# Optimization experiments

Hardware: AMD Instinct MI355X
Metric: run time of the kernel (lower is better)

The kernel has to match this reference:

```python
import jax, jax.numpy as jnp
import numpy as np

OUT_FEATURES = 4096
IN_FEATURES = 4096
R = 16
DIST = 4
N_FREQ = 10000
SCALING = 150.0


def setup_inputs() -> dict:
    key = jax.random.key(0)
    k_x, k_w, k_b, k_s, k_a, k_i = jax.random.split(key, 6)
    x = jax.random.normal(k_x, (4, 2048, IN_FEATURES), dtype=jnp.float32)
    base_w = jax.random.normal(k_w, (OUT_FEATURES, IN_FEATURES), dtype=jnp.float32) * 0.02
    base_b = jax.random.normal(k_b, (OUT_FEATURES,), dtype=jnp.float32) * 0.02
    spectrum = jax.random.normal(k_s, (N_FREQ,), dtype=jnp.float32)
    hora_A = jax.random.normal(k_a, (R, IN_FEATURES), dtype=jnp.float32)
    # torch uses randperm(r*out_features)[:n_frequency] -> unique flat indices
    idx = jax.random.permutation(k_i, R * OUT_FEATURES)[:N_FREQ].astype(jnp.int32)
    return {"x": x, "base_w": base_w, "base_b": base_b,
            "spectrum": spectrum, "hora_A": hora_A, "idx": idx}


def reference(x, base_w, base_b, spectrum, hora_A, idx):
    # --- get_delta_weight ---
    rows = idx // R            # index into out_features
    cols = idx % R             # index into r
    dense_spectrum = jnp.zeros((OUT_FEATURES, R), dtype=spectrum.dtype)
    dense_spectrum = dense_spectrum.at[rows, cols].set(spectrum)
    # chunk_size = ceil(out/dist) = 1024; out divisible by dist -> pure reshape
    chunks = dense_spectrum.reshape(DIST, OUT_FEATURES // DIST, R)
    B = jnp.fft.ifft2(chunks, axes=(-2, -1)).real.astype(spectrum.dtype)
    B = B.reshape(OUT_FEATURES, R)
    delta_w = (B * SCALING) @ hora_A          # [out_features, in_features]
    # --- forward: base linear + adapter linear ---
    base_out = jnp.einsum('bsi,oi->bso', x, base_w) + base_b
    result = base_out + jnp.einsum('bsi,oi->bso', x, delta_w)
    return result
```

## Files before the change

kernel.cpp:

```cpp
#include <hip/hip_runtime.h>
#include <hip/hip_bf16.h>


#define OUTF 4096
#define INF  4096
#define NFREQ 10000
#define MDIM 8192
#define KT   (INF / 64)
#define NX4  ((MDIM * INF) / 4)

typedef __attribute__((ext_vector_type(8))) short bf16x8;
typedef __attribute__((ext_vector_type(4))) float f32x4;

__device__ __forceinline__ unsigned int bf16pack2(float a, float b) {
    unsigned int ua = __builtin_bit_cast(unsigned int, a);
    unsigned int ub = __builtin_bit_cast(unsigned int, b);
    ua = (ua + 0x7fffu + ((ua >> 16) & 1u)) >> 16;
    ub = (ub + 0x7fffu + ((ub >> 16) & 1u)) & 0xffff0000u;
    return ua | ub;
}

__device__ __forceinline__ void async_copy16(const void* g, void* l) {
    __builtin_amdgcn_global_load_lds(
        (__attribute__((address_space(1))) void*)(g),
        (__attribute__((address_space(3))) void*)(l),
        16, 0, 0);
}

__global__ __launch_bounds__(256) void k1_compact_cvt_kernel(
        const float* __restrict__ spectrum, const int* __restrict__ idx,
        int2* __restrict__ cjk2, int* __restrict__ boff,
        const float4* __restrict__ x4, uint2* __restrict__ xb) {
    __shared__ int2 s_list[4096];
    __shared__ int  wcnt[4];
    __shared__ int  s_cnt;
    __shared__ int  kcnt[16];
    __shared__ int  kbase[17];
    const int tid = threadIdx.x;
    if (blockIdx.x >= 4) {
        for (int i = (blockIdx.x - 4) * 256 + tid; i < NX4; i += 2044 * 256) {
            float4 v = x4[i];
            xb[i] = make_uint2(bf16pack2(v.x, v.y), bf16pack2(v.z, v.w));
        }
        return;
    }
    const int p  = blockIdx.x;
    const int wv = tid >> 6, ln = tid & 63;
    int cnt = 0;
    for (int i0 = wv * 64; i0 < NFREQ; i0 += 256) {
        const int i = i0 + ln;
        bool m = (i < NFREQ) && ((idx[i] >> 14) == p);
        cnt += __popcll(__ballot(m));
    }
    if (ln == 0) wcnt[wv] = cnt;
    __syncthreads();
    int base = 0;
    for (int w = 0; w < wv; ++w) base += wcnt[w];
    for (int i0 = wv * 64; i0 < NFREQ; i0 += 256) {
        const int i = i0 + ln;
        bool m = false; int id = 0;
        if (i < NFREQ) { id = idx[i]; m = ((id >> 14) == p); }
        unsigned long long bal = __ballot(m);
        if (m) {
            int pos = base + __popcll(bal & ((1ull << ln) - 1ull));
            if (pos < 4096)
                s_list[pos] = make_int2(id & 16383,
                                        __builtin_bit_cast(int, spectrum[i]));
        }
        base += __popcll(bal);
    }
    if (tid == 0) {
        int t = wcnt[0] + wcnt[1] + wcnt[2] + wcnt[3];
        s_cnt = (t < 4096) ? t : 4096;
    }
    __syncthreads();
    const int n = s_cnt;
    for (int q = 0; q < 4; ++q) {
        const int k = wv * 4 + q;
        int c = 0;
        for (int t0 = 0; t0 < n; t0 += 64) {
            const int t = t0 + ln;
            bool m = (t < n) && ((s_list[t].x & 15) == k);
            c += __popcll(__ballot(m));
        }
        if (ln == 0) kcnt[k] = c;
    }
    __syncthreads();
    if (tid == 0) {
        int a = 0;
        for (int k = 0; k < 16; ++k) { kbase[k] = a; a += kcnt[k]; }
        kbase[16] = a;
    }
    __syncthreads();
    for (int q = 0; q < 4; ++q) {
        const int k = wv * 4 + q;
        int b2 = kbase[k];
        for (int t0 = 0; t0 < n; t0 += 64) {
            const int t = t0 + ln;
            bool m = (t < n) && ((s_list[t].x & 15) == k);
            unsigned long long bal = __ballot(m);
            if (m) {
                int pos = b2 + __popcll(bal & ((1ull << ln) - 1ull));
                cjk2[p * 4096 + pos] = make_int2(s_list[t].x >> 4, s_list[t].y);
            }
            b2 += __popcll(bal);
        }
    }
    if (tid < 17) boff[p * 17 + tid] = kbase[tid];
}

__global__ __launch_bounds__(256) void k2_w_kernel(
        const int2* __restrict__ cjk2, const int* __restrict__ boff,
        const float* __restrict__ bw, const float* __restrict__ A,
        unsigned short* __restrict__ W) {
    __shared__ int2  s_jv[4096];
    __shared__ float s1re[8][16];
    __shared__ float s1im[8][17];
    __shared__ float sB[8][17];
    const int tid = threadIdx.x;
    const int n0  = blockIdx.x * 8;
    const int p   = n0 >> 10;
    const int cnt = boff[p * 17 + 16];
    for (int t = tid; t < cnt; t += 256) s_jv[t] = cjk2[p * 4096 + t];
    __syncthreads();
    if (tid < 128) {
        const int m_loc = tid >> 4;
        const int k     = tid & 15;
        const int m     = (n0 & 1023) + m_loc;
        const int kb0   = boff[p * 17 + k];
        const int kb1   = boff[p * 17 + k + 1];
        const float c1  = 6.283185307179586f / 1024.f;
        float re = 0.f, im = 0.f;
        for (int t = kb0; t < kb1; ++t) {
            const int2 jv = s_jv[t];
            const float v = __builtin_bit_cast(float, jv.y);
            const float ang = (float)((jv.x * m) & 1023) * c1;
            re += v * __cosf(ang);
            im += v * __sinf(ang);
        }
        s1re[m_loc][k] = re;
        s1im[m_loc][k] = im;
    }
    __syncthreads();
    if (tid < 128) {
        const int m_loc = tid >> 4;
        const int r     = tid & 15;
        const float c2  = 6.283185307179586f / 16.f;
        float b = 0.f;
#pragma unroll
        for (int k2 = 0; k2 < 16; ++k2) {
            const float ang = (float)((k2 * r) & 15) * c2;
            b += s1re[m_loc][k2] * __cosf(ang) - s1im[m_loc][k2] * __sinf(ang);
        }
        sB[m_loc][r] = b * (150.f / 16384.f);
    }
    __syncthreads();
    const float4* A4  = (const float4*)A;
    const float4* bw4 = (const float4*)bw;
    uint2* W2 = (uint2*)W;
#pragma unroll 1
    for (int q = 0; q < 4; ++q) {
        const int c4 = tid + q * 256;
        float4 a[16];
#pragma unroll
        for (int r = 0; r < 16; ++r) a[r] = A4[r * 1024 + c4];
#pragma unroll 1
        for (int nn = 0; nn < 8; ++nn) {
            const int n = n0 + nn;
            float4 wv = bw4[n * 1024 + c4];
#pragma unroll
            for (int r = 0; r < 16; ++r) {
                float s = sB[nn][r];
                wv.x += s * a[r].x; wv.y += s * a[r].y;
                wv.z += s * a[r].z; wv.w += s * a[r].w;
            }
            W2[n * 1024 + c4] = make_uint2(bf16pack2(wv.x, wv.y),
                                           bf16pack2(wv.z, wv.w));
        }
    }
}

__global__ __launch_bounds__(512, 2) void gemm256_kernel(
        const unsigned short* __restrict__ Xb,
        const unsigned short* __restrict__ Wb,
        const float* __restrict__ bias, float* __restrict__ C) {
    __shared__ __align__(1024) char lds[131072];

    const int tid  = threadIdx.x;
    const int lane = tid & 63;
    const int wid  = tid >> 6;
    const int wm   = wid >> 2;
    const int wn   = wid & 3;

    int bid = blockIdx.x;
    bid = (bid & 7) * 64 + (bid >> 3);
    const int tm = bid >> 4;
    const int tn = bid & 15;
    const int arow0 = tm * 256;
    const int brow0 = tn * 256;

    const int srow  = tid >> 3;
    const int scole = (((tid & 7) * 16) ^ ((srow & 7) << 4)) >> 1;
    const int sldsb = tid * 16;

    const int l15 = lane & 15;
    const int kx0 = ((lane >> 4) * 16) ^ ((lane & 7) << 4);
    const int kx1 = kx0 ^ 64;
    const int abase0 = (wm * 128 + l15) * 128;
    const int bbase0 = 32768 + (wn * 64 + l15) * 128;

    f32x4 acc[8][4] = {};
    bf16x8 af[4][2], bfa[2][2], bfb[2][2];

#define STAGE_HALF(mat, grow0, t, ldsbase) do {                               \
        const unsigned short* _s =                                            \
            (mat) + ((grow0) + srow) * INF + (t) * 64 + scole;                \
        async_copy16(_s, lds + (ldsbase) + sldsb);                            \
        async_copy16(_s + 64 * INF, lds + (ldsbase) + 8192 + sldsb);          \
    } while (0)

#define LDA(DB, m, kh) (*(const bf16x8*)(lds + (DB) + abase0 + (m) * 2048 + ((kh) ? kx1 : kx0)))
#define LDB(DB, n, kh) (*(const bf16x8*)(lds + (DB) + bbase0 + (n) * 2048 + ((kh) ? kx1 : kx0)))
#define MFMA(a, b, c) __builtin_amdgcn_mfma_f32_16x16x32_bf16((a), (b), (c), 0, 0, 0)
#define BARRIER() do { asm volatile("" ::: "memory");                         \
                       __builtin_amdgcn_s_barrier();                          \
                       asm volatile("" ::: "memory"); } while (0)
#define LGKM0()  asm volatile("s_waitcnt lgkmcnt(0)" ::: "memory")

#define QMFMA(mh, BF)                                                         \
    __builtin_amdgcn_s_setprio(1);                                            \
    _Pragma("unroll") for (int ks = 0; ks < 2; ++ks)                          \
        _Pragma("unroll") for (int m = 0; m < 4; ++m)                         \
            _Pragma("unroll") for (int n = 0; n < 2; ++n)                     \
                acc[(mh) * 4 + m][(BF) * 2 + n] =                             \
                    MFMA(af[m][ks], ((BF) ? bfb : bfa)[n][ks],                \
                         acc[(mh) * 4 + m][(BF) * 2 + n]);                    \
    __builtin_amdgcn_s_setprio(0)

#define RD_AF(DB, mh)                                                         \
    _Pragma("unroll") for (int m = 0; m < 4; ++m) {                           \
        af[m][0] = LDA(DB, (mh) * 4 + m, 0);                                  \
        af[m][1] = LDA(DB, (mh) * 4 + m, 1); }
#define RD_BFA(DB)                                                            \
    _Pragma("unroll") for (int n = 0; n < 2; ++n) {                           \
        bfa[n][0] = LDB(DB, n, 0); bfa[n][1] = LDB(DB, n, 1); }
#define RD_BFB(DB)                                                            \
    _Pragma("unroll") for (int n = 0; n < 2; ++n) {                           \
        bfb[n][0] = LDB(DB, n + 2, 0); bfb[n][1] = LDB(DB, n + 2, 1); }

#define PAIR(CUR, OTH, s) do {                                                \
    RD_AF(CUR, 0);                                                            \
    STAGE_HALF(Xb, arow0 + 128, (s) + 1, (OTH) + 16384);                      \
    BARRIER(); LGKM0(); QMFMA(0, 0); BARRIER();                               \
    RD_BFB(CUR);                                                              \
    STAGE_HALF(Wb, brow0 + 128, (s) + 1, (OTH) + 49152);                      \
    BARRIER(); LGKM0(); QMFMA(0, 1); BARRIER();                               \
    RD_AF(CUR, 1);                                                            \
    if ((s) + 2 < KT) STAGE_HALF(Wb, brow0, (s) + 2, (CUR) + 32768);          \
    BARRIER(); LGKM0(); QMFMA(1, 0); BARRIER();                               \
    if ((s) + 2 < KT) {                                                       \
        STAGE_HALF(Xb, arow0, (s) + 2, (CUR) + 0);                            \
        asm volatile("s_waitcnt vmcnt(4)" ::: "memory");                      \
    } else { asm volatile("s_waitcnt vmcnt(0)" ::: "memory"); }               \
    BARRIER();                                                                \
    RD_BFA(OTH);                                                              \
    QMFMA(1, 1); BARRIER();                                                   \
    RD_AF(OTH, 0);                                                            \
    if ((s) + 2 < KT) STAGE_HALF(Xb, arow0 + 128, (s) + 2, (CUR) + 16384);    \
    BARRIER(); LGKM0(); QMFMA(0, 0); BARRIER();                               \
    RD_BFB(OTH);                                                              \
    if ((s) + 2 < KT) STAGE_HALF(Wb, brow0 + 128, (s) + 2, (CUR) + 49152);    \
    BARRIER(); LGKM0(); QMFMA(0, 1); BARRIER();                               \
    RD_AF(OTH, 1);                                                            \
    if ((s) + 3 < KT) STAGE_HALF(Wb, brow0, (s) + 3, (OTH) + 32768);          \
    BARRIER(); LGKM0(); QMFMA(1, 0); BARRIER();                               \
    if ((s) + 3 < KT) {                                                       \
        STAGE_HALF(Xb, arow0, (s) + 3, (OTH) + 0);                            \
        asm volatile("s_waitcnt vmcnt(4)" ::: "memory");                      \
    } else { asm volatile("s_waitcnt vmcnt(0)" ::: "memory"); }               \
    BARRIER();                                                                \
    if ((s) + 2 < KT) { RD_BFA(CUR); }                                        \
    QMFMA(1, 1); BARRIER();                                                   \
} while (0)

    STAGE_HALF(Wb, brow0,       0, 32768);
    STAGE_HALF(Xb, arow0,       0, 0);
    STAGE_HALF(Xb, arow0 + 128, 0, 16384);
    STAGE_HALF(Wb, brow0 + 128, 0, 49152);
    STAGE_HALF(Wb, brow0,       1, 65536 + 32768);
    STAGE_HALF(Xb, arow0,       1, 65536 + 0);
    asm volatile("s_waitcnt vmcnt(4)" ::: "memory");
    BARRIER();
    RD_BFA(0);

    for (int s = 0; s < KT; s += 2)
        PAIR(0, 65536, s);

#pragma unroll
    for (int n = 0; n < 4; ++n) {
        const int gcol = brow0 + wn * 64 + n * 16 + l15;
        const float bv = bias[gcol];
#pragma unroll
        for (int m = 0; m < 8; ++m) {
            const int grow = arow0 + wm * 128 + m * 16 + (lane >> 4) * 4;
#pragma unroll
            for (int rg = 0; rg < 4; ++rg)
                C[(grow + rg) * OUTF + gcol] = acc[m][n][rg] + bv;
        }
    }
#undef STAGE_HALF
#undef LDA
#undef LDB
#undef MFMA
#undef BARRIER
#undef LGKM0
#undef QMFMA
#undef RD_AF
#undef RD_BFA
#undef RD_BFB
#undef PAIR
}

extern "C" void kernel_launch(void* const* d_in, const int* in_sizes, int n_in,
                              void* d_out, int out_size, void* d_ws, size_t ws_size,
                              hipStream_t stream) {
    const float* x    = (const float*)d_in[0];
    const float* bw   = (const float*)d_in[1];
    const float* bb   = (const float*)d_in[2];
    const float* spec = (const float*)d_in[3];
    const float* ha   = (const float*)d_in[4];
    const int*   idx  = (const int*)d_in[5];
    float* out = (float*)d_out;

    char* ws = (char*)d_ws;
    unsigned short* Wb   = (unsigned short*)ws;
    unsigned short* Xb   = (unsigned short*)(ws + 33554432);
    int2*           cjk2 = (int2*)(ws + 100663296);
    int*            boff = (int*)(ws + 100794368);

    k1_compact_cvt_kernel<<<2048, 256, 0, stream>>>(
        spec, idx, cjk2, boff, (const float4*)x, (uint2*)Xb);
    k2_w_kernel<<<512, 256, 0, stream>>>(cjk2, boff, bw, ha, Wb);
    gemm256_kernel<<<512, 512, 0, stream>>>(Xb, Wb, bb, out);
}
```

Baseline: 379.4 us.

## Cut barriers in GEMM main loop and overlap last MFMA quarter with staging

Removes the leading barrier before each MFMA quarter in the ping-pong K loop, leaving one barrier per quarter. The last quarter now issues its MFMAs before the vmcnt wait instead of after it, and the B-fragment read for the next buffer moves to the start of the next half-iteration. This is meant to cut synchronisation stalls and hide global-load latency behind compute. Fewer barriers raise the risk of LDS read/write races between waves if any remaining ordering is insufficient.

```diff
diff --git a/kernel.cpp b/kernel.cpp
--- a/kernel.cpp
+++ b/kernel.cpp
@@ -249,38 +249,42 @@
         bfb[n][0] = LDB(DB, n + 2, 0); bfb[n][1] = LDB(DB, n + 2, 1); }
 
 #define PAIR(CUR, OTH, s) do {                                                \
-    RD_AF(CUR, 0);                                                            \
+                                    \
+    RD_AF(CUR, 0); RD_BFA(CUR);                                               \
     STAGE_HALF(Xb, arow0 + 128, (s) + 1, (OTH) + 16384);                      \
-    BARRIER(); LGKM0(); QMFMA(0, 0); BARRIER();                               \
+    LGKM0(); QMFMA(0, 0); BARRIER();                                          \
+                                            \
     RD_BFB(CUR);                                                              \
     STAGE_HALF(Wb, brow0 + 128, (s) + 1, (OTH) + 49152);                      \
-    BARRIER(); LGKM0(); QMFMA(0, 1); BARRIER();                               \
+    LGKM0(); QMFMA(0, 1); BARRIER();                                          \
+                                      \
     RD_AF(CUR, 1);                                                            \
     if ((s) + 2 < KT) STAGE_HALF(Wb, brow0, (s) + 2, (CUR) + 32768);          \
-    BARRIER(); LGKM0(); QMFMA(1, 0); BARRIER();                               \
-    if ((s) + 2 < KT) {                                                       \
-        STAGE_HALF(Xb, arow0, (s) + 2, (CUR) + 0);                            \
-        asm volatile("s_waitcnt vmcnt(4)" ::: "memory");                      \
-    } else { asm volatile("s_waitcnt vmcnt(0)" ::: "memory"); }               \
+    LGKM0(); QMFMA(1, 0); BARRIER();                                          \
+                \
+    if ((s) + 2 < KT) STAGE_HALF(Xb, arow0, (s) + 2, (CUR) + 0);              \
+    QMFMA(1, 1);                                                              \
+    if ((s) + 2 < KT) { asm volatile("s_waitcnt vmcnt(4)" ::: "memory"); }    \
+    else              { asm volatile("s_waitcnt vmcnt(0)" ::: "memory"); }    \
     BARRIER();                                                                \
-    RD_BFA(OTH);                                                              \
-    QMFMA(1, 1); BARRIER();                                                   \
-    RD_AF(OTH, 0);                                                            \
+                               \
+    RD_AF(OTH, 0); RD_BFA(OTH);                                               \
     if ((s) + 2 < KT) STAGE_HALF(Xb, arow0 + 128, (s) + 2, (CUR) + 16384);    \
-    BARRIER(); LGKM0(); QMFMA(0, 0); BARRIER();                               \
+    LGKM0(); QMFMA(0, 0); BARRIER();                                          \
+                                       \
     RD_BFB(OTH);                                                              \
     if ((s) + 2 < KT) STAGE_HALF(Wb, brow0 + 128, (s) + 2, (CUR) + 49152);    \
-    BARRIER(); LGKM0(); QMFMA(0, 1); BARRIER();                               \
+    LGKM0(); QMFMA(0, 1); BARRIER();                                          \
+                                      \
     RD_AF(OTH, 1);                                                            \
     if ((s) + 3 < KT) STAGE_HALF(Wb, brow0, (s) + 3, (OTH) + 32768);          \
-    BARRIER(); LGKM0(); QMFMA(1, 0); BARRIER();                               \
-    if ((s) + 3 < KT) {                                                       \
-        STAGE_HALF(Xb, arow0, (s) + 3, (OTH) + 0);                            \
-        asm volatile("s_waitcnt vmcnt(4)" ::: "memory");                      \
-    } else { asm volatile("s_waitcnt vmcnt(0)" ::: "memory"); }               \
+    LGKM0(); QMFMA(1, 0); BARRIER();                                          \
+              \
+    if ((s) + 3 < KT) STAGE_HALF(Xb, arow0, (s) + 3, (OTH) + 0);              \
+    QMFMA(1, 1);                                                              \
+    if ((s) + 3 < KT) { asm volatile("s_waitcnt vmcnt(4)" ::: "memory"); }    \
+    else              { asm volatile("s_waitcnt vmcnt(0)" ::: "memory"); }    \
     BARRIER();                                                                \
-    if ((s) + 2 < KT) { RD_BFA(CUR); }                                        \
-    QMFMA(1, 1); BARRIER();                                                   \
 } while (0)
 
     STAGE_HALF(Wb, brow0,       0, 32768);
@@ -291,7 +295,6 @@
     STAGE_HALF(Xb, arow0,       1, 65536 + 0);
     asm volatile("s_waitcnt vmcnt(4)" ::: "memory");
     BARRIER();
-    RD_BFA(0);
 
     for (int s = 0; s < KT; s += 2)
         PAIR(0, 65536, s);
```

Measured after the change: 377.0 us. Within noise of the previous version (-0.6%).
